# Kernel optimization log

Measured on AMD Instinct MI355X. Metric: run time of the kernel, lower is better.

The kernel has to match this reference:

```python
import jax, jax.numpy as jnp
import numpy as np

MARGIN = 0.3
PD_EPS = 1e-6  # torch F.pairwise_distance adds eps to the difference


def setup_inputs() -> dict:
    key = jax.random.key(0)
    k1, k2 = jax.random.split(key)
    B, D, NUM_CLASSES = 8192, 256, 8
    embeddings = jax.random.normal(k1, (B, D), dtype=jnp.float32)
    labels = jax.random.randint(k2, (B,), 0, NUM_CLASSES, dtype=jnp.int64)
    return {"embeddings": embeddings, "labels": labels}


def _pairwise_euclidean(x):
    # cdist(x, x, p=2) via the Gram trick; clamp tiny negatives before sqrt
    sq = jnp.sum(x * x, axis=1)  # [B]
    d2 = sq[:, None] + sq[None, :] - 2.0 * (x @ x.T)
    return jnp.sqrt(jnp.maximum(d2, 0.0))


def reference(embeddings, labels):
    B = embeddings.shape[0]
    D = _pairwise_euclidean(embeddings)  # [B, B]

    eq = labels[:, None] == labels[None, :]
    eye = jnp.eye(B, dtype=bool)
    pos_mask = eq & ~eye          # same label, not self
    neg_mask = ~eq                # different label

    # hard mining: per anchor, farthest positive and closest negative
    pos_idx = jnp.argmax(jnp.where(pos_mask, D, -jnp.inf), axis=1)  # [B]
    neg_idx = jnp.argmin(jnp.where(neg_mask, D, jnp.inf), axis=1)   # [B]
    valid = pos_mask.any(axis=1) & neg_mask.any(axis=1)             # [B]

    # recompute triplet distances like F.pairwise_distance (eps on the diff)
    pos_dist = jnp.linalg.norm(embeddings - embeddings[pos_idx] + PD_EPS, axis=1)
    neg_dist = jnp.linalg.norm(embeddings - embeddings[neg_idx] + PD_EPS, axis=1)

    per_anchor = jax.nn.relu(pos_dist - neg_dist + MARGIN)
    n_valid = jnp.maximum(valid.sum(), 1)
    loss = jnp.sum(jnp.where(valid, per_anchor, 0.0)) / n_valid.astype(per_anchor.dtype)
    return loss
```

## Files before the change

kernel.cpp:

```cpp
#include <hip/hip_runtime.h>
#include <math.h>


typedef __attribute__((ext_vector_type(8))) short short8;
typedef __attribute__((ext_vector_type(4))) float floatx4;

#define B_N 8192
#define D_K 256

__device__ __forceinline__ unsigned short f2bf_rne(float f) {
  unsigned u = __float_as_uint(f);
  u += 0x7FFFu + ((u >> 16) & 1u);
  return (unsigned short)(u >> 16);
}

#define DPP_SHR(x, CTRL) \
  ((unsigned)__builtin_amdgcn_update_dpp((int)(x), (int)(x), (CTRL), 0xF, 0xF, false))

__global__ void k_hist(const int* __restrict__ lab, int* __restrict__ chunkhist) {
  __shared__ int h[8];
  const int tid = threadIdx.x, b = blockIdx.x;
  if (tid < 8) h[tid] = 0;
  __syncthreads();
  atomicAdd(&h[lab[b * 256 + tid] & 7], 1);
  __syncthreads();
  if (tid < 8) chunkhist[b * 8 + tid] = h[tid];
}

__global__ void k_perm(const int* __restrict__ lab, const int* __restrict__ chunkhist,
                       int* __restrict__ perm, int* __restrict__ labp) {
  __shared__ int ch[256];
  __shared__ int base[8];
  __shared__ int wcnt[4][8];
  const int tid = threadIdx.x, b = blockIdx.x;
  ch[tid] = chunkhist[tid];
  __syncthreads();
  if (tid < 8) {
    const int c = tid;
    int acc = 0;
    for (int cc = 0; cc < c; ++cc)
      for (int k = 0; k < 32; ++k) acc += ch[k * 8 + cc];
    for (int k = 0; k < b; ++k) acc += ch[k * 8 + c];
    base[c] = acc;
  }
  const int i    = b * 256 + tid;
  const int myc  = lab[i] & 7;
  const int lane = tid & 63, w = tid >> 6;
  unsigned long long bal[8];
#pragma unroll
  for (int c = 0; c < 8; ++c) bal[c] = __ballot(myc == c);
  if (lane == 0) {
#pragma unroll
    for (int c = 0; c < 8; ++c) wcnt[w][c] = (int)__popcll(bal[c]);
  }
  __syncthreads();
  int rank = (int)__popcll(bal[myc] & ((1ull << lane) - 1ull));
  for (int ww = 0; ww < w; ++ww) rank += wcnt[ww][myc];
  const int pos = base[myc] + rank;
  perm[pos] = i;
  labp[pos] = myc;
}

__global__ void k_split(const float* __restrict__ x, const int* __restrict__ perm,
                        unsigned short* __restrict__ xhf,
                        float* __restrict__ sqq,
                        float* __restrict__ sum, int* __restrict__ cnt,
                        int* __restrict__ done) {
  __shared__ float sw[64];
  const int tid  = threadIdx.x;
  const int lane = tid & 63;
  const int w    = tid >> 6;
  const int b    = blockIdx.x;
  const int m    = lane & 15;
  const int quad = lane >> 4;
  const int row  = b * 16 + m;
  const int rsrc = perm[row];

  float s = 0.f;
#pragma unroll
  for (int h = 0; h < 2; ++h) {
    int tk = w + h * 4;
    int kk = tk * 32 + quad * 8;
    float4 f0 = *reinterpret_cast<const float4*>(x + (size_t)rsrc * D_K + kk);
    float4 f1 = *reinterpret_cast<const float4*>(x + (size_t)rsrc * D_K + kk + 4);
    s += f0.x * f0.x + f0.y * f0.y + f0.z * f0.z + f0.w * f0.w;
    s += f1.x * f1.x + f1.y * f1.y + f1.z * f1.z + f1.w * f1.w;
    ushort4 lo, hi;
    lo.x = f2bf_rne(f0.x); lo.y = f2bf_rne(f0.y); lo.z = f2bf_rne(f0.z); lo.w = f2bf_rne(f0.w);
    hi.x = f2bf_rne(f1.x); hi.y = f2bf_rne(f1.y); hi.z = f2bf_rne(f1.z); hi.w = f2bf_rne(f1.w);
    size_t o = ((size_t)b * 8 + tk) * 512 + lane * 8;
    *reinterpret_cast<ushort4*>(xhf + o)     = lo;
    *reinterpret_cast<ushort4*>(xhf + o + 4) = hi;
  }
  s += __shfl_xor(s, 16);
  s += __shfl_xor(s, 32);
  if (quad == 0) sw[w * 16 + m] = s;
  __syncthreads();
  if (tid < 16) {
    int i = b * 16 + tid;
    float t = sw[tid] + sw[16 + tid] + sw[32 + tid] + sw[48 + tid];
    sqq[i] = fmaf(t, 128.f, 262144.f);
  }
  if (b == 0 && tid == 0) { *sum = 0.f; *cnt = 0; *done = 0; }
}

template <int MODE>
__device__ __forceinline__ void mine_tail(
    const floatx4* acc, const int* __restrict__ labp, const float* __restrict__ sqq,
    const float* sqi, int i0, int bi, int bj, int hb, int w, int lane,
    unsigned* jbp, unsigned* jbn,
    unsigned* __restrict__ ppart, unsigned* __restrict__ npart) {
  const int wi = w >> 1, wj = w & 1;
  const int quad = lane >> 4, l15 = lane & 15;

  unsigned lip = 0;
  if (MODE == 2) {
#pragma unroll
    for (int r = 0; r < 8; ++r) {
      int ir = i0 + (r >> 2) * 16 + quad * 4 + (r & 3);
      lip |= ((unsigned)labp[ir] & 0xFu) << (r * 4);
    }
  }

  unsigned pkey[8], nkey[8];
#pragma unroll
  for (int r = 0; r < 8; ++r) { pkey[r] = 0u; nkey[r] = 0xFFFFFFFFu; }

#pragma unroll
  for (int nt = 0; nt < 4; ++nt) {
    int      j  = bj * 128 + wj * 64 + nt * 16 + l15;
    float    sj = sqq[j];
    unsigned jl = (MODE == 2) ? ((unsigned)labp[j] & 0xFu) : 0u;
    unsigned jp = 0u, jn = 0xFFFFFFFFu;
#pragma unroll
    for (int r = 0; r < 8; ++r) {
      float dot = acc[(r >> 2) * 4 + nt][r & 3];
      int   ir  = i0 + (r >> 2) * 16 + quad * 4 + (r & 3);
      unsigned keyi = ((unsigned)fmaf(-256.f, dot, sj) << 13) | (unsigned)j;
      unsigned keyj = ((unsigned)fmaf(-256.f, dot, sqi[r]) << 13) | (unsigned)ir;
      if (MODE == 2) {
        bool eq = (jl == ((lip >> (r * 4)) & 0xFu));
        unsigned pci = eq ? keyi : 0u;
        unsigned nci = eq ? 0xFFFFFFFFu : keyi;
        pkey[r] = pkey[r] > pci ? pkey[r] : pci;
        nkey[r] = nkey[r] < nci ? nkey[r] : nci;
        unsigned pcj = eq ? keyj : 0u;
        unsigned ncj = eq ? 0xFFFFFFFFu : keyj;
        jp = jp > pcj ? jp : pcj;
        jn = jn < ncj ? jn : ncj;
      } else if (MODE == 1) {
        pkey[r] = pkey[r] > keyi ? pkey[r] : keyi;
        jp = jp > keyj ? jp : keyj;
      } else {
        nkey[r] = nkey[r] < keyi ? nkey[r] : keyi;
        jn = jn < keyj ? jn : keyj;
      }
    }
#pragma unroll
    for (int m = 16; m < 64; m <<= 1) {
      if (MODE != 0) {
        unsigned op = (unsigned)__shfl_xor((int)jp, m);
        jp = jp > op ? jp : op;
      }
      if (MODE != 1) {
        unsigned on = (unsigned)__shfl_xor((int)jn, m);
        jn = jn < on ? jn : on;
      }
    }
    if (quad == 0) {
      if (MODE != 0) jbp[w * 64 + nt * 16 + l15] = jp;
      if (MODE != 1) jbn[w * 64 + nt * 16 + l15] = jn;
    }
  }

#pragma unroll
  for (int r = 0; r < 8; ++r) {
    if (MODE != 0) { unsigned tp = DPP_SHR(pkey[r], 0x118); pkey[r] = pkey[r] > tp ? pkey[r] : tp; }
    if (MODE != 1) { unsigned tn = DPP_SHR(nkey[r], 0x118); nkey[r] = nkey[r] < tn ? nkey[r] : tn; }
  }
#pragma unroll
  for (int r = 0; r < 8; ++r) {
    if (MODE != 0) { unsigned tp = DPP_SHR(pkey[r], 0x114); pkey[r] = pkey[r] > tp ? pkey[r] : tp; }
    if (MODE != 1) { unsigned tn = DPP_SHR(nkey[r], 0x114); nkey[r] = nkey[r] < tn ? nkey[r] : tn; }
  }
#pragma unroll
  for (int r = 0; r < 8; ++r) {
    if (MODE != 0) { unsigned tp = DPP_SHR(pkey[r], 0x112); pkey[r] = pkey[r] > tp ? pkey[r] : tp; }
    if (MODE != 1) { unsigned tn = DPP_SHR(nkey[r], 0x112); nkey[r] = nkey[r] < tn ? nkey[r] : tn; }
  }
#pragma unroll
  for (int r = 0; r < 8; ++r) {
    if (MODE != 0) { unsigned tp = DPP_SHR(pkey[r], 0x111); pkey[r] = pkey[r] > tp ? pkey[r] : tp; }
    if (MODE != 1) { unsigned tn = DPP_SHR(nkey[r], 0x111); nkey[r] = nkey[r] < tn ? nkey[r] : tn; }
  }
#pragma unroll
  for (int r = 0; r < 8; ++r) {
    if (l15 == 15) {
      int ir = i0 + (r >> 2) * 16 + quad * 4 + (r & 3);
      size_t idx = (size_t)(2 * bj + wj) * B_N + ir;
      ppart[idx] = (MODE == 0) ? 0u : pkey[r];
      npart[idx] = (MODE == 1) ? 0xFFFFFFFFu : nkey[r];
    }
  }

  __syncthreads();
  if (wi == 0 && bi != bj) {
    unsigned p = 0u, n = 0xFFFFFFFFu;
    if (MODE != 0) {
      p = jbp[w * 64 + lane];
      unsigned p2 = jbp[(w + 2) * 64 + lane];
      p = p > p2 ? p : p2;
    }
    if (MODE != 1) {
      n = jbn[w * 64 + lane];
      unsigned n2 = jbn[(w + 2) * 64 + lane];
      n = n < n2 ? n : n2;
    }
    int j = bj * 128 + wj * 64 + lane;
    size_t idx = (size_t)(2 * bi + hb) * B_N + j;
    ppart[idx] = p;
    npart[idx] = n;
  }
}

__global__ __launch_bounds__(256, 6) void k_mine16(
    const unsigned short* __restrict__ xhf, const int* __restrict__ labp,
    const float* __restrict__ sqq,
    unsigned* __restrict__ ppart, unsigned* __restrict__ npart) {
  __shared__ unsigned jbp[4 * 64], jbn[4 * 64];

  int t  = blockIdx.x;
  const int hb = t & 1;
  t >>= 1;
  int bi = (int)(64.5f - sqrtf(64.5f * 64.5f - 2.f * (float)t));
  int b0 = 64 * bi - (bi * (bi - 1)) / 2;
  if (t < b0) { bi--; b0 = 64 * bi - (bi * (bi - 1)) / 2; }
  else {
    int b1 = 64 * (bi + 1) - ((bi + 1) * bi) / 2;
    if (t >= b1) { bi++; b0 = b1; }
  }
  const int bj = bi + (t - b0);

  const int tid  = threadIdx.x;
  const int lane = tid & 63;
  const int w    = tid >> 6;
  const int wi   = w >> 1;
  const int wj   = w & 1;
  const int quad = lane >> 4;
  const int i0   = bi * 128 + hb * 64 + wi * 32;

  float sqi[8];
#pragma unroll
  for (int r = 0; r < 8; ++r)
    sqi[r] = sqq[i0 + (r >> 2) * 16 + quad * 4 + (r & 3)];

  const int la0 = labp[bi * 128 + hb * 64];
  const int la1 = labp[bi * 128 + hb * 64 + 63];
  const int lb0 = labp[bj * 128];
  const int lb1 = labp[bj * 128 + 127];

  const unsigned aoff = (unsigned)(i0 >> 4) * 4096u + (unsigned)lane * 8u;
  const unsigned boff = (unsigned)(bj * 8 + wj * 4) * 4096u + (unsigned)lane * 8u;

  floatx4 acc[8];
#pragma unroll
  for (int q = 0; q < 8; ++q) acc[q] = (floatx4)0.f;

#pragma unroll
  for (int tk = 0; tk < 8; ++tk) {
    short8 Bf[4];
#pragma unroll
    for (int nt = 0; nt < 4; ++nt)
      Bf[nt] = *reinterpret_cast<const short8*>(xhf + boff + (unsigned)(nt * 4096 + tk * 512));
    short8 Af[2];
#pragma unroll
    for (int mt = 0; mt < 2; ++mt)
      Af[mt] = *reinterpret_cast<const short8*>(xhf + aoff + (unsigned)(mt * 8 + tk) * 512u);
#pragma unroll
    for (int mt = 0; mt < 2; ++mt)
#pragma unroll
      for (int nt = 0; nt < 4; ++nt)
        acc[mt * 4 + nt] = __builtin_amdgcn_mfma_f32_16x16x32_bf16(
            Af[mt], Bf[nt], acc[mt * 4 + nt], 0, 0, 0);
  }

  if (la1 < lb0 || lb1 < la0) {
    mine_tail<0>(acc, labp, sqq, sqi, i0, bi, bj, hb, w, lane, jbp, jbn, ppart, npart);
  } else if (la0 == lb1 && la1 == lb0) {
    mine_tail<1>(acc, labp, sqq, sqi, i0, bi, bj, hb, w, lane, jbp, jbn, ppart, npart);
  } else {
    mine_tail<2>(acc, labp, sqq, sqi, i0, bi, bj, hb, w, lane, jbp, jbn, ppart, npart);
  }
}

__global__ void k_finish(const float* __restrict__ x, const int* __restrict__ perm,
                         const unsigned* __restrict__ ppart,
                         const unsigned* __restrict__ npart,
                         float* __restrict__ sum, int* __restrict__ cnt,
                         int* __restrict__ done, float* __restrict__ out) {
  __shared__ unsigned spk[32], snk[32];
  __shared__ float ssum[4];
  __shared__ int   scnt[4];
  const int tid = threadIdx.x;
  const int a0  = blockIdx.x * 32;

  if (tid < 32) { spk[tid] = 0u; snk[tid] = 0xFFFFFFFFu; }
  __syncthreads();

  {
    const int a    = a0 + (tid & 31);
    const int part = tid >> 5;
    unsigned p = 0u, n = 0xFFFFFFFFu;
#pragma unroll
    for (int s = 0; s < 16; ++s) {
      size_t idx = (size_t)(part * 16 + s) * B_N + a;
      unsigned pv = ppart[idx];
      unsigned nv = npart[idx];
      p = p > pv ? p : pv;
      n = n < nv ? n : nv;
    }
    atomicMax(&spk[tid & 31], p);
    atomicMin(&snk[tid & 31], n);
  }
  __syncthreads();

  const int w = tid >> 6, lane = tid & 63;
  float lsum = 0.f; int lcnt = 0;
#pragma unroll
  for (int it = 0; it < 8; ++it) {
    int al = w * 8 + it;
    int a  = a0 + al;
    unsigned p = spk[al];
    unsigned n = snk[al];
    bool valid = (p != 0u) && (n != 0xFFFFFFFFu);
    int  pidx = valid ? (int)(p & 8191u) : 0;
    int  nidx = valid ? (int)(n & 8191u) : 0;
    int  ra = perm[a], rp = perm[pidx], rn = perm[nidx];

    float4 xa = *reinterpret_cast<const float4*>(x + (size_t)ra * D_K + lane * 4);
    float4 xp = *reinterpret_cast<const float4*>(x + (size_t)rp * D_K + lane * 4);
    float4 xn = *reinterpret_cast<const float4*>(x + (size_t)rn * D_K + lane * 4);
    float dx, sp = 0.f, sn = 0.f;
    dx = xa.x - xp.x + 1e-6f; sp = fmaf(dx, dx, sp);
    dx = xa.y - xp.y + 1e-6f; sp = fmaf(dx, dx, sp);
    dx = xa.z - xp.z + 1e-6f; sp = fmaf(dx, dx, sp);
    dx = xa.w - xp.w + 1e-6f; sp = fmaf(dx, dx, sp);
    dx = xa.x - xn.x + 1e-6f; sn = fmaf(dx, dx, sn);
    dx = xa.y - xn.y + 1e-6f; sn = fmaf(dx, dx, sn);
    dx = xa.z - xn.z + 1e-6f; sn = fmaf(dx, dx, sn);
    dx = xa.w - xn.w + 1e-6f; sn = fmaf(dx, dx, sn);
#pragma unroll
    for (int o = 32; o > 0; o >>= 1) {
      sp += __shfl_down(sp, o, 64);
      sn += __shfl_down(sn, o, 64);
    }
    if (lane == 0 && valid) {
      float per = sqrtf(sp) - sqrtf(sn) + 0.3f;
      if (per > 0.f) lsum += per;
      lcnt += 1;
    }
  }
  if (lane == 0) { ssum[w] = lsum; scnt[w] = lcnt; }
  __syncthreads();
  if (tid == 0) {
    atomicAdd(sum, ssum[0] + ssum[1] + ssum[2] + ssum[3]);
    atomicAdd(cnt, scnt[0] + scnt[1] + scnt[2] + scnt[3]);
    __threadfence();
    int prev = atomicAdd(done, 1);
    if (prev == gridDim.x - 1) {
      float s = atomicAdd(sum, 0.f);
      int   cc = atomicAdd(cnt, 0);
      if (cc < 1) cc = 1;
      out[0] = s / (float)cc;
    }
  }
}

extern "C" void kernel_launch(void* const* d_in, const int* in_sizes, int n_in,
                              void* d_out, int out_size, void* d_ws, size_t ws_size,
                              hipStream_t stream) {
  const float* x   = (const float*)d_in[0];
  const int*   lab = (const int*)d_in[1];
  float*       out = (float*)d_out;

  char* ws = (char*)d_ws;
  unsigned short* xhf = (unsigned short*)ws;
  int* perm      = (int*)(ws + (size_t)4096 * 1024);
  int* labp      = (int*)(ws + (size_t)4096 * 1024 + 32768);
  int* chunkhist = (int*)(ws + (size_t)4096 * 1024 + 65536);
  float* sqq = (float*)(ws + (size_t)4608 * 1024);
  char*  pb = ws + (size_t)4608 * 1024 + 65536;
  size_t seg = (size_t)128 * B_N * 4;
  unsigned* ppart = (unsigned*)(pb);
  unsigned* npart = (unsigned*)(pb + seg);
  float* sum  = (float*)(pb + 2 * seg);
  int*   cnt  = (int*)(sum + 1);
  int*   done = (int*)(sum + 2);

  k_hist<<<32, 256, 0, stream>>>(lab, chunkhist);
  k_perm<<<32, 256, 0, stream>>>(lab, chunkhist, perm, labp);
  k_split<<<B_N / 16, 256, 0, stream>>>(x, perm, xhf, sqq, sum, cnt, done);
  k_mine16<<<4160, 256, 0, stream>>>(xhf, labp, sqq, ppart, npart);
  k_finish<<<B_N / 32, 256, 0, stream>>>(x, perm, ppart, npart, sum, cnt, done, out);
}
```

Before: 124.4 us.

## Enlarge mining tile to full 128x128 per block, halving grid

Each block of the pairwise mining kernel now covers a full 128x128 tile instead of a 64-row half-tile. Each warp computes a 64x64 sub-block with 16 MFMA accumulators, and the launch count drops from 4160 to 2080. The aim is to reuse B-fragment loads across more rows and cut per-block overhead and column-reduction partial writes. In exchange register pressure doubles, so launch bounds fall to 3 blocks per SM, which lowers occupancy. The column-partial writes are also restructured to fill the now-unused half slot with identity values.

New measurement: 118.4 us. 1.05x faster.

```diff
diff --git a/kernel.cpp b/kernel.cpp
--- a/kernel.cpp
+++ b/kernel.cpp
@@ -107,39 +107,44 @@
 template <int MODE>
 __device__ __forceinline__ void mine_tail(
     const floatx4* acc, const int* __restrict__ labp, const float* __restrict__ sqq,
-    const float* sqi, int i0, int bi, int bj, int hb, int w, int lane,
+    int i0, int bi, int bj, int w, int lane,
     unsigned* jbp, unsigned* jbn,
     unsigned* __restrict__ ppart, unsigned* __restrict__ npart) {
-  const int wi = w >> 1, wj = w & 1;
+  const int wj = w & 1;
   const int quad = lane >> 4, l15 = lane & 15;
 
-  unsigned lip = 0;
+  float sqi[16];
+#pragma unroll
+  for (int r = 0; r < 16; ++r)
+    sqi[r] = sqq[i0 + (r >> 2) * 16 + quad * 4 + (r & 3)];
+
+  unsigned long long lip = 0ull;
   if (MODE == 2) {
 #pragma unroll
-    for (int r = 0; r < 8; ++r) {
+    for (int r = 0; r < 16; ++r) {
       int ir = i0 + (r >> 2) * 16 + quad * 4 + (r & 3);
-      lip |= ((unsigned)labp[ir] & 0xFu) << (r * 4);
-    }
-  }
-
-  unsigned pkey[8], nkey[8];
-#pragma unroll
-  for (int r = 0; r < 8; ++r) { pkey[r] = 0u; nkey[r] = 0xFFFFFFFFu; }
+      lip |= (unsigned long long)((unsigned)labp[ir] & 0xFu) << (r * 4);
+    }
+  }
+
+  unsigned pkey[16], nkey[16];
+#pragma unroll
+  for (int r = 0; r < 16; ++r) { pkey[r] = 0u; nkey[r] = 0xFFFFFFFFu; }
 
 #pragma unroll
   for (int nt = 0; nt < 4; ++nt) {
-    int      j  = bj * 128 + wj * 64 + nt * 16 + l15;
-    float    sj = sqq[j];
-    unsigned jl = (MODE == 2) ? ((unsigned)labp[j] & 0xFu) : 0u;
+    const int      j  = bj * 128 + wj * 64 + nt * 16 + l15;
+    const float    sj = sqq[j];
+    const unsigned jl = (MODE == 2) ? ((unsigned)labp[j] & 0xFu) : 0u;
     unsigned jp = 0u, jn = 0xFFFFFFFFu;
 #pragma unroll
-    for (int r = 0; r < 8; ++r) {
+    for (int r = 0; r < 16; ++r) {
       float dot = acc[(r >> 2) * 4 + nt][r & 3];
       int   ir  = i0 + (r >> 2) * 16 + quad * 4 + (r & 3);
       unsigned keyi = ((unsigned)fmaf(-256.f, dot, sj) << 13) | (unsigned)j;
       unsigned keyj = ((unsigned)fmaf(-256.f, dot, sqi[r]) << 13) | (unsigned)ir;
       if (MODE == 2) {
-        bool eq = (jl == ((lip >> (r * 4)) & 0xFu));
+        bool eq = (jl == (unsigned)((lip >> (r * 4)) & 0xFull));
         unsigned pci = eq ? keyi : 0u;
         unsigned nci = eq ? 0xFFFFFFFFu : keyi;
         pkey[r] = pkey[r] > pci ? pkey[r] : pci;
@@ -158,14 +163,8 @@
     }
 #pragma unroll
     for (int m = 16; m < 64; m <<= 1) {
-      if (MODE != 0) {
-        unsigned op = (unsigned)__shfl_xor((int)jp, m);
-        jp = jp > op ? jp : op;
-      }
-      if (MODE != 1) {
-        unsigned on = (unsigned)__shfl_xor((int)jn, m);
-        jn = jn < on ? jn : on;
-      }
+      if (MODE != 0) { unsigned op = (unsigned)__shfl_xor((int)jp, m); jp = jp > op ? jp : op; }
+      if (MODE != 1) { unsigned on = (unsigned)__shfl_xor((int)jn, m); jn = jn < on ? jn : on; }
     }
     if (quad == 0) {
       if (MODE != 0) jbp[w * 64 + nt * 16 + l15] = jp;
@@ -174,27 +173,27 @@
   }
 
 #pragma unroll
-  for (int r = 0; r < 8; ++r) {
+  for (int r = 0; r < 16; ++r) {
     if (MODE != 0) { unsigned tp = DPP_SHR(pkey[r], 0x118); pkey[r] = pkey[r] > tp ? pkey[r] : tp; }
     if (MODE != 1) { unsigned tn = DPP_SHR(nkey[r], 0x118); nkey[r] = nkey[r] < tn ? nkey[r] : tn; }
   }
 #pragma unroll
-  for (int r = 0; r < 8; ++r) {
+  for (int r = 0; r < 16; ++r) {
     if (MODE != 0) { unsigned tp = DPP_SHR(pkey[r], 0x114); pkey[r] = pkey[r] > tp ? pkey[r] : tp; }
     if (MODE != 1) { unsigned tn = DPP_SHR(nkey[r], 0x114); nkey[r] = nkey[r] < tn ? nkey[r] : tn; }
   }
 #pragma unroll
-  for (int r = 0; r < 8; ++r) {
+  for (int r = 0; r < 16; ++r) {
     if (MODE != 0) { unsigned tp = DPP_SHR(pkey[r], 0x112); pkey[r] = pkey[r] > tp ? pkey[r] : tp; }
     if (MODE != 1) { unsigned tn = DPP_SHR(nkey[r], 0x112); nkey[r] = nkey[r] < tn ? nkey[r] : tn; }
   }
 #pragma unroll
-  for (int r = 0; r < 8; ++r) {
+  for (int r = 0; r < 16; ++r) {
     if (MODE != 0) { unsigned tp = DPP_SHR(pkey[r], 0x111); pkey[r] = pkey[r] > tp ? pkey[r] : tp; }
     if (MODE != 1) { unsigned tn = DPP_SHR(nkey[r], 0x111); nkey[r] = nkey[r] < tn ? nkey[r] : tn; }
   }
 #pragma unroll
-  for (int r = 0; r < 8; ++r) {
+  for (int r = 0; r < 16; ++r) {
     if (l15 == 15) {
       int ir = i0 + (r >> 2) * 16 + quad * 4 + (r & 3);
       size_t idx = (size_t)(2 * bj + wj) * B_N + ir;
@@ -204,7 +203,7 @@
   }
 
   __syncthreads();
-  if (wi == 0 && bi != bj) {
+  if ((w >> 1) == 0 && bi != bj) {
     unsigned p = 0u, n = 0xFFFFFFFFu;
     if (MODE != 0) {
       p = jbp[w * 64 + lane];
@@ -217,21 +216,20 @@
       n = n < n2 ? n : n2;
     }
     int j = bj * 128 + wj * 64 + lane;
-    size_t idx = (size_t)(2 * bi + hb) * B_N + j;
-    ppart[idx] = p;
-    npart[idx] = n;
-  }
-}
-
-__global__ __launch_bounds__(256, 6) void k_mine16(
+    size_t v = (size_t)(2 * bi + wj)       * B_N + j;
+    size_t u = (size_t)(2 * bi + (1 - wj)) * B_N + j;
+    ppart[v] = p;   npart[v] = n;
+    ppart[u] = 0u;  npart[u] = 0xFFFFFFFFu;
+  }
+}
+
+__global__ __launch_bounds__(256, 3) void k_mine16(
     const unsigned short* __restrict__ xhf, const int* __restrict__ labp,
     const float* __restrict__ sqq,
     unsigned* __restrict__ ppart, unsigned* __restrict__ npart) {
   __shared__ unsigned jbp[4 * 64], jbn[4 * 64];
 
   int t  = blockIdx.x;
-  const int hb = t & 1;
-  t >>= 1;
   int bi = (int)(64.5f - sqrtf(64.5f * 64.5f - 2.f * (float)t));
   int b0 = 64 * bi - (bi * (bi - 1)) / 2;
   if (t < b0) { bi--; b0 = 64 * bi - (bi * (bi - 1)) / 2; }
@@ -246,25 +244,19 @@
   const int w    = tid >> 6;
   const int wi   = w >> 1;
   const int wj   = w & 1;
-  const int quad = lane >> 4;
-  const int i0   = bi * 128 + hb * 64 + wi * 32;
-
-  float sqi[8];
-#pragma unroll
-  for (int r = 0; r < 8; ++r)
-    sqi[r] = sqq[i0 + (r >> 2) * 16 + quad * 4 + (r & 3)];
-
-  const int la0 = labp[bi * 128 + hb * 64];
-  const int la1 = labp[bi * 128 + hb * 64 + 63];
+  const int i0   = bi * 128 + wi * 64;
+
+  const int la0 = labp[bi * 128];
+  const int la1 = labp[bi * 128 + 127];
   const int lb0 = labp[bj * 128];
   const int lb1 = labp[bj * 128 + 127];
 
-  const unsigned aoff = (unsigned)(i0 >> 4) * 4096u + (unsigned)lane * 8u;
+  const unsigned aoff = (unsigned)(bi * 8 + wi * 4) * 4096u + (unsigned)lane * 8u;
   const unsigned boff = (unsigned)(bj * 8 + wj * 4) * 4096u + (unsigned)lane * 8u;
 
-  floatx4 acc[8];
-#pragma unroll
-  for (int q = 0; q < 8; ++q) acc[q] = (floatx4)0.f;
+  floatx4 acc[16];
+#pragma unroll
+  for (int q = 0; q < 16; ++q) acc[q] = (floatx4)0.f;
 
 #pragma unroll
   for (int tk = 0; tk < 8; ++tk) {
@@ -272,12 +264,12 @@
 #pragma unroll
     for (int nt = 0; nt < 4; ++nt)
       Bf[nt] = *reinterpret_cast<const short8*>(xhf + boff + (unsigned)(nt * 4096 + tk * 512));
-    short8 Af[2];
-#pragma unroll
-    for (int mt = 0; mt < 2; ++mt)
-      Af[mt] = *reinterpret_cast<const short8*>(xhf + aoff + (unsigned)(mt * 8 + tk) * 512u);
-#pragma unroll
-    for (int mt = 0; mt < 2; ++mt)
+    short8 Af[4];
+#pragma unroll
+    for (int mt = 0; mt < 4; ++mt)
+      Af[mt] = *reinterpret_cast<const short8*>(xhf + aoff + (unsigned)(mt * 4096 + tk * 512));
+#pragma unroll
+    for (int mt = 0; mt < 4; ++mt)
 #pragma unroll
       for (int nt = 0; nt < 4; ++nt)
         acc[mt * 4 + nt] = __builtin_amdgcn_mfma_f32_16x16x32_bf16(
@@ -285,11 +277,11 @@
   }
 
   if (la1 < lb0 || lb1 < la0) {
-    mine_tail<0>(acc, labp, sqq, sqi, i0, bi, bj, hb, w, lane, jbp, jbn, ppart, npart);
+    mine_tail<0>(acc, labp, sqq, i0, bi, bj, w, lane, jbp, jbn, ppart, npart);
   } else if (la0 == lb1 && la1 == lb0) {
-    mine_tail<1>(acc, labp, sqq, sqi, i0, bi, bj, hb, w, lane, jbp, jbn, ppart, npart);
+    mine_tail<1>(acc, labp, sqq, i0, bi, bj, w, lane, jbp, jbn, ppart, npart);
   } else {
-    mine_tail<2>(acc, labp, sqq, sqi, i0, bi, bj, hb, w, lane, jbp, jbn, ppart, npart);
+    mine_tail<2>(acc, labp, sqq, i0, bi, bj, w, lane, jbp, jbn, ppart, npart);
   }
 }
 
@@ -400,6 +392,6 @@
   k_hist<<<32, 256, 0, stream>>>(lab, chunkhist);
   k_perm<<<32, 256, 0, stream>>>(lab, chunkhist, perm, labp);
   k_split<<<B_N / 16, 256, 0, stream>>>(x, perm, xhf, sqq, sum, cnt, done);
-  k_mine16<<<4160, 256, 0, stream>>>(xhf, labp, sqq, ppart, npart);
+  k_mine16<<<2080, 256, 0, stream>>>(xhf, labp, sqq, ppart, npart);
   k_finish<<<B_N / 32, 256, 0, stream>>>(x, perm, ppart, npart, sum, cnt, done, out);
 }
```
